# Kernel optimization log

Measured on AMD Instinct MI355X. Metric: run time of the kernel, lower is better.

## Reference

```python
import jax, jax.numpy as jnp
import numpy as np

B, T, NE, NZ, H = 64, 1024, 256, 64, 256  # batch, timesteps, n_e, n_z, encoder_hidden
SW_HID = 128  # switch MLP hidden width (hardcoded in source)


def setup_inputs() -> dict:
    key = jax.random.key(0)
    ks = jax.random.split(key, 16)
    s = 0.05
    p = lambda k, shape: (jax.random.normal(k, shape, dtype=jnp.float32) * s)
    return {
        "e_seq": jax.random.normal(ks[0], (B, T, NE), dtype=jnp.float32),
        "eps": jax.random.normal(ks[1], (B, T, NZ), dtype=jnp.float32),  # randn_like noise, precomputed
        # GRU forward direction (torch layout: weight_ih [3H, NE] order r,z,n)
        "w_ih_f": p(ks[2], (3 * H, NE)), "w_hh_f": p(ks[3], (3 * H, H)),
        "b_ih_f": jnp.zeros((3 * H,), jnp.float32), "b_hh_f": jnp.zeros((3 * H,), jnp.float32),
        # GRU backward direction
        "w_ih_b": p(ks[4], (3 * H, NE)), "w_hh_b": p(ks[5], (3 * H, H)),
        "b_ih_b": jnp.zeros((3 * H,), jnp.float32), "b_hh_b": jnp.zeros((3 * H,), jnp.float32),
        # mu / logvar heads over [B,T,2H]
        "mu_w": p(ks[6], (NZ, 2 * H)), "mu_b": jnp.zeros((NZ,), jnp.float32),
        "lv_w": p(ks[7], (NZ, 2 * H)), "lv_b": jnp.zeros((NZ,), jnp.float32),
        # switching unit: Linear(NE + 2H + NZ, 128) -> ReLU -> Linear(128,1) -> Sigmoid
        "sw_w1": p(ks[8], (SW_HID, NE + 2 * H + NZ)), "sw_b1": jnp.zeros((SW_HID,), jnp.float32),
        "sw_w2": p(ks[9], (1, SW_HID)), "sw_b2": jnp.zeros((1,), jnp.float32),
    }


def _gru_dir(x, w_ih, w_hh, b_ih, b_hh, reverse):
    # x: [B,T,NE]; torch GRU cell: r,z = sigmoid; n = tanh(x_n + r*(W_hn h + b_hn)); h' = (1-z)*n + z*h
    xp = jnp.einsum('btn,gn->btg', x, w_ih) + b_ih  # [B,T,3H] input projections, once
    xp = jnp.swapaxes(xp, 0, 1)  # [T,B,3H]
    h0 = jnp.zeros((x.shape[0], w_hh.shape[1]), x.dtype)

    def step(h, xpt):
        hp = h @ w_hh.T + b_hh
        xr, xz, xn = jnp.split(xpt, 3, axis=-1)
        hr, hz, hn = jnp.split(hp, 3, axis=-1)
        r = jax.nn.sigmoid(xr + hr)
        z = jax.nn.sigmoid(xz + hz)
        n = jnp.tanh(xn + r * hn)
        h_new = (1.0 - z) * n + z * h
        return h_new, h_new

    _, hs = jax.lax.scan(step, h0, xp, reverse=reverse)  # outputs time-aligned even when reversed
    return jnp.swapaxes(hs, 0, 1)  # [B,T,H]


def _forward(e_seq, eps, w_ih_f, w_hh_f, b_ih_f, b_hh_f, w_ih_b, w_hh_b, b_ih_b, b_hh_b,
             mu_w, mu_b, lv_w, lv_b, sw_w1, sw_b1, sw_w2, sw_b2):
    h_f = _gru_dir(e_seq, w_ih_f, w_hh_f, b_ih_f, b_hh_f, reverse=False)
    h_b = _gru_dir(e_seq, w_ih_b, w_hh_b, b_ih_b, b_hh_b, reverse=True)
    h_seq = jnp.concatenate([h_f, h_b], axis=-1)  # [B,T,2H]

    mu = h_seq @ mu_w.T + mu_b    # [B,T,NZ]
    lv = h_seq @ lv_w.T + lv_b    # [B,T,NZ]

    n_e = e_seq.shape[-1]
    h2 = h_seq.shape[-1]
    # split switch first-layer weight by input segments [e_t | h_t | z_prev]
    w1_e = sw_w1[:, :n_e]
    w1_h = sw_w1[:, n_e:n_e + h2]
    w1_z = sw_w1[:, n_e + h2:]
    # precompute e/h contributions for all t; only z_prev contribution is sequential
    pre = jnp.einsum('btn,kn->btk', e_seq, w1_e) + jnp.einsum('bth,kh->btk', h_seq, w1_h) + sw_b1  # [B,T,128]

    z_tilde = mu + jnp.exp(0.5 * lv) * eps                    # reparameterized sample [B,T,NZ]
    kl = (-0.5 * (1.0 + lv - mu * mu - jnp.exp(lv))).sum(-1)  # [B,T]

    def step(z_prev, inputs):
        pre_t, zt_t = inputs  # [B,128], [B,NZ]
        hid = jax.nn.relu(pre_t + z_prev @ w1_z.T)
        beta = jax.nn.sigmoid(hid @ sw_w2.T + sw_b2)[..., 0]  # [B]
        z_t = beta[:, None] * zt_t + (1.0 - beta[:, None]) * z_prev
        return z_t, (z_t, beta)

    z0 = jnp.zeros((e_seq.shape[0], mu.shape[-1]), e_seq.dtype)
    _, (zs, betas) = jax.lax.scan(step, z0, (jnp.swapaxes(pre, 0, 1), jnp.swapaxes(z_tilde, 0, 1)))
    z_seq = jnp.swapaxes(zs, 0, 1)     # [B,T,NZ]
    beta_seq = jnp.swapaxes(betas, 0, 1)  # [B,T]
    kl_loss = kl.mean()
    return z_seq, kl_loss, beta_seq


def reference(e_seq, eps, w_ih_f, w_hh_f, b_ih_f, b_hh_f, w_ih_b, w_hh_b, b_ih_b, b_hh_b,
              mu_w, mu_b, lv_w, lv_b, sw_w1, sw_b1, sw_w2, sw_b2):
    return _forward(e_seq, eps, w_ih_f, w_hh_f, b_ih_f, b_hh_f, w_ih_b, w_hh_b, b_ih_b, b_hh_b,
                    mu_w, mu_b, lv_w, lv_b, sw_w1, sw_b1, sw_w2, sw_b2)
```

## Files before the change

kernel.cpp:

```cpp
#include <hip/hip_runtime.h>
#include <cstdint>

typedef _Float16 half_t;
typedef _Float16 half2_t __attribute__((ext_vector_type(2)));
typedef _Float16 h8_t __attribute__((ext_vector_type(8)));
typedef float f4_t __attribute__((ext_vector_type(4)));
typedef unsigned int uint32;

static constexpr int B_ = 64, T_ = 1024;

#define DEV __device__ __forceinline__

DEV float fdot2f(half2_t a, half2_t b, float c) {
#if __has_builtin(__builtin_amdgcn_fdot2)
  return __builtin_amdgcn_fdot2(a, b, c, false);
#else
  return fmaf((float)a.x, (float)b.x, fmaf((float)a.y, (float)b.y, c));
#endif
}

DEV float fast_rcp(float x) { return __builtin_amdgcn_rcpf(x); }
DEV float sigmf(float x) { return fast_rcp(1.f + __expf(-x)); }
DEV float tanhf_(float x) { return 1.f - 2.f * fast_rcp(1.f + __expf(2.f * x)); }
DEV uint32 pack2(float a, float b) {
  half2_t h; h.x = (half_t)a; h.y = (half_t)b;
  return __builtin_bit_cast(uint32, h);
}

DEV void gload_lds16(const void* g, void* l) {
  __builtin_amdgcn_global_load_lds(
      (const __attribute__((address_space(1))) uint32*)g,
      (__attribute__((address_space(3))) uint32*)l, 16, 0, 0);
}

__global__ __launch_bounds__(256) void pack_w(
    const float* __restrict__ w_ih_f, const float* __restrict__ w_ih_b,
    const float* __restrict__ mu_w, const float* __restrict__ lv_w,
    const float* __restrict__ sw_w1,
    const float* __restrict__ w_hh_f, const float* __restrict__ w_hh_b,
    const float* __restrict__ mu_b, const float* __restrict__ lv_b,
    const float* __restrict__ sw_b1,
    uint32* __restrict__ wihf, uint32* __restrict__ wihb,
    uint32* __restrict__ wce, uint32* __restrict__ wchf, uint32* __restrict__ wchb,
    uint32* __restrict__ whh, uint32* __restrict__ w1z, float* __restrict__ biasc) {
  int id = blockIdx.x * 256 + threadIdx.x;
  if (id < 98304) { wihf[id] = pack2(w_ih_f[2*id], w_ih_f[2*id+1]); return; }
  id -= 98304;
  if (id < 98304) { wihb[id] = pack2(w_ih_b[2*id], w_ih_b[2*id+1]); return; }
  id -= 98304;
  if (id < 32768) {
    int n = id >> 7, c0 = (id & 127) * 2;
    float v0 = 0.f, v1 = 0.f;
    if (n >= 128) { const float* p = sw_w1 + (n - 128) * 832 + c0; v0 = p[0]; v1 = p[1]; }
    wce[id] = pack2(v0, v1); return;
  }
  id -= 32768;
  if (id < 32768) {
    int n = id >> 7, c0 = (id & 127) * 2;
    const float* p = (n < 64)  ? mu_w + n * 512 + c0
                   : (n < 128) ? lv_w + (n - 64) * 512 + c0
                               : sw_w1 + (n - 128) * 832 + 256 + c0;
    wchf[id] = pack2(p[0], p[1]); return;
  }
  id -= 32768;
  if (id < 32768) {
    int n = id >> 7, c0 = (id & 127) * 2;
    const float* p = (n < 64)  ? mu_w + n * 512 + 256 + c0
                   : (n < 128) ? lv_w + (n - 64) * 512 + 256 + c0
                               : sw_w1 + (n - 128) * 832 + 512 + c0;
    wchb[id] = pack2(p[0], p[1]); return;
  }
  id -= 32768;
  if (id < 196608) {
    int d = id / 98304, q = id % 98304;
    int dw = q / 512, t2 = q % 512;
    int r = t2 >> 2, pp = t2 & 3;
    int i = dw / 96, g = (dw % 96) / 32, dd = dw % 32;
    int row = 256 * g + 2 * r + i;
    int k0 = 64 * pp + 2 * dd;
    const float* w = d ? w_hh_b : w_hh_f;
    whh[id] = pack2(w[row * 256 + k0], w[row * 256 + k0 + 1]);
    return;
  }
  id -= 196608;
  if (id < 4096) {
    int j = id / 128, k2 = id % 128;
    w1z[id] = pack2(sw_w1[k2 * 832 + 768 + 2 * j], sw_w1[k2 * 832 + 768 + 2 * j + 1]);
    return;
  }
  id -= 4096;
  if (id < 256) {
    biasc[id] = (id < 64) ? mu_b[id] : (id < 128) ? lv_b[id - 64] : sw_b1[id - 128];
  }
}

template <int AF32, int ACC>
__global__ __launch_bounds__(256) void gemm_t(
    const void* __restrict__ Ap, int lda,
    const half_t* __restrict__ Bw,
    const float* __restrict__ bias,
    half_t* __restrict__ C, int ldc, int K) {
  __shared__ __align__(16) half_t smem[16384];
  half_t* As = smem;
  half_t* Bs = smem + 8192;
  const int tid = threadIdx.x;
  const int lane = tid & 63, w = tid >> 6;
  const int n0 = blockIdx.x * 128, m0 = blockIdx.y * 128;
  const int r8 = lane >> 3, c8 = lane & 7;
  f4_t acc[4][4];
  f4_t zero = {0.f, 0.f, 0.f, 0.f};
#pragma unroll
  for (int i = 0; i < 4; ++i)
#pragma unroll
    for (int j = 0; j < 4; ++j) acc[i][j] = zero;
  const int wm = (w >> 1) * 64, wn = (w & 1) * 64;
  for (int ks = 0; ks < K; ks += 64) {
    if constexpr (AF32) {
      const float* Af = (const float*)Ap;
#pragma unroll
      for (int it = 0; it < 4; ++it) {
        int c = it * 256 + tid;
        int row = c >> 3, coff = (c & 7) * 8;
        const float* ap = Af + (size_t)(m0 + row) * lda + ks + coff;
        float4 v0 = *(const float4*)ap;
        float4 v1 = *(const float4*)(ap + 4);
        uint4 u;
        u.x = pack2(v0.x, v0.y); u.y = pack2(v0.z, v0.w);
        u.z = pack2(v1.x, v1.y); u.w = pack2(v1.z, v1.w);
        *(uint4*)&As[(size_t)c * 8] = u;
      }
    } else {
      const half_t* Af = (const half_t*)Ap;
#pragma unroll
      for (int c = 0; c < 4; ++c) {
        int row = w * 32 + c * 8 + r8;
        gload_lds16(Af + (size_t)(m0 + row) * lda + ks + c8 * 8, As + (w * 4 + c) * 512);
      }
    }
#pragma unroll
    for (int c = 0; c < 4; ++c) {
      int row = w * 32 + c * 8 + r8;
      gload_lds16(Bw + (size_t)(n0 + row) * K + ks + c8 * 8, Bs + (w * 4 + c) * 512);
    }
    __syncthreads();
#pragma unroll
    for (int kk = 0; kk < 2; ++kk) {
      h8_t af[4], bf[4];
      const int ko = kk * 32 + (lane >> 4) * 8;
#pragma unroll
      for (int i = 0; i < 4; ++i) af[i] = *(const h8_t*)&As[(wm + i * 16 + (lane & 15)) * 64 + ko];
#pragma unroll
      for (int j = 0; j < 4; ++j) bf[j] = *(const h8_t*)&Bs[(wn + j * 16 + (lane & 15)) * 64 + ko];
#pragma unroll
      for (int i = 0; i < 4; ++i)
#pragma unroll
        for (int j = 0; j < 4; ++j)
          acc[i][j] = __builtin_amdgcn_mfma_f32_16x16x32_f16(af[i], bf[j], acc[i][j], 0, 0, 0);
    }
    __syncthreads();
  }
  const int cl4 = lane & 15, rl4 = lane >> 4;
#pragma unroll
  for (int j = 0; j < 4; ++j) {
    float bj = bias ? bias[n0 + wn + j * 16 + cl4] : 0.f;
#pragma unroll
    for (int i = 0; i < 4; ++i)
#pragma unroll
      for (int q = 0; q < 4; ++q) {
        int rl = wm + i * 16 + rl4 * 4 + q;
        int cc = wn + j * 16 + cl4;
        smem[rl * 128 + cc] = (half_t)(acc[i][j][q] + bj);
      }
  }
  __syncthreads();
#pragma unroll
  for (int it = 0; it < 8; ++it) {
    int idx = it * 256 + tid;
    int row = idx >> 4, colc = idx & 15;
    uint4 v = *(const uint4*)&smem[row * 128 + colc * 8];
    half_t* cp = C + (size_t)(m0 + row) * ldc + n0 + colc * 8;
    if constexpr (ACC) {
      uint4 o = *(const uint4*)cp;
      h8_t vv = __builtin_bit_cast(h8_t, v) + __builtin_bit_cast(h8_t, o);
      v = __builtin_bit_cast(uint4, vv);
    }
    *(uint4*)cp = v;
  }
}

__global__ __launch_bounds__(512, 2) void gru_rec(
    uint32* __restrict__ xp,
    const uint32* __restrict__ whh,
    const float* __restrict__ bhh_f, const float* __restrict__ bhh_b) {
  const int wg = blockIdx.x;
  const int d = wg >> 6, b = wg & 63;
  const int tid = threadIdx.x;
  const int r = tid >> 2, p = tid & 3;
  __shared__ uint32 hb[2][128];
  if (tid < 128) { hb[0][tid] = 0; hb[1][tid] = 0; }
  half2_t wv[192];
  const uint32* wp = whh + (size_t)d * 98304 + tid;
#pragma unroll
  for (int j = 0; j < 192; ++j) wv[j] = __builtin_bit_cast(half2_t, wp[j * 512]);
  const float* bhh = d ? bhh_b : bhh_f;
  float bh[6];
#pragma unroll
  for (int g = 0; g < 3; ++g) { bh[g] = bhh[256 * g + 2 * r]; bh[3 + g] = bhh[256 * g + 2 * r + 1]; }
  uint32* xpu = xp + ((size_t)d * B_ + b) * T_ * 384;
  float h0 = 0.f, h1 = 0.f;
  const int dt = d ? -1 : 1;
  int t = d ? (T_ - 1) : 0;
  uint32 xr_n = 0, xz_n = 0, xn_n = 0;
  if (p == 0) {
    const uint32* rowp = xpu + (size_t)t * 384;
    xr_n = rowp[r]; xz_n = rowp[128 + r]; xn_n = rowp[256 + r];
  }
  __syncthreads();
  for (int step = 0; step < T_; ++step) {
    const int cur = step & 1;
    const uint32 xr = xr_n, xz = xz_n, xn = xn_n;
    const int tn = (step < T_ - 1) ? (t + dt) : t;
    if (p == 0) {
      const uint32* rowp = xpu + (size_t)tn * 384;
      xr_n = rowp[r]; xz_n = rowp[128 + r]; xn_n = rowp[256 + r];
    }
    float a00 = 0, a01 = 0, a02 = 0, a10 = 0, a11 = 0, a12 = 0;
#pragma unroll
    for (int c = 0; c < 4; ++c) {
      half2_t hv[8];
#pragma unroll
      for (int e = 0; e < 8; ++e) hv[e] = __builtin_bit_cast(half2_t, hb[cur][p * 32 + c * 8 + e]);
#pragma unroll
      for (int e = 0; e < 8; ++e) {
        const int dd = c * 8 + e;
        a00 = fdot2f(wv[dd], hv[e], a00);
        a01 = fdot2f(wv[dd + 32], hv[e], a01);
        a02 = fdot2f(wv[dd + 64], hv[e], a02);
        a10 = fdot2f(wv[dd + 96], hv[e], a10);
        a11 = fdot2f(wv[dd + 128], hv[e], a11);
        a12 = fdot2f(wv[dd + 160], hv[e], a12);
      }
    }
    a00 += __shfl_xor(a00, 1); a00 += __shfl_xor(a00, 2);
    a01 += __shfl_xor(a01, 1); a01 += __shfl_xor(a01, 2);
    a02 += __shfl_xor(a02, 1); a02 += __shfl_xor(a02, 2);
    a10 += __shfl_xor(a10, 1); a10 += __shfl_xor(a10, 2);
    a11 += __shfl_xor(a11, 1); a11 += __shfl_xor(a11, 2);
    a12 += __shfl_xor(a12, 1); a12 += __shfl_xor(a12, 2);
    if (p == 0) {
      half2_t xrv = __builtin_bit_cast(half2_t, xr);
      half2_t xzv = __builtin_bit_cast(half2_t, xz);
      half2_t xnv = __builtin_bit_cast(half2_t, xn);
      float r0 = sigmf((float)xrv.x + a00 + bh[0]);
      float z0 = sigmf((float)xzv.x + a01 + bh[1]);
      float n0 = tanhf_((float)xnv.x + r0 * (a02 + bh[2]));
      h0 = (1.f - z0) * n0 + z0 * h0;
      float r1 = sigmf((float)xrv.y + a10 + bh[3]);
      float z1 = sigmf((float)xzv.y + a11 + bh[4]);
      float n1 = tanhf_((float)xnv.y + r1 * (a12 + bh[5]));
      h1 = (1.f - z1) * n1 + z1 * h1;
      uint32 ph = pack2(h0, h1);
      hb[cur ^ 1][r] = ph;
      xpu[(size_t)t * 384 + r] = ph;
    }
    __syncthreads();
    t = tn;
  }
}

__global__ __launch_bounds__(256) void zkl(const half_t* __restrict__ hp,
                                           const float* __restrict__ eps,
                                           float* __restrict__ ztil,
                                           float* __restrict__ klp) {
  const int blk = blockIdx.x, tid = threadIdx.x;
  const size_t bt = (size_t)blk * 4 + (tid >> 6);
  const int j = tid & 63;
  float mu = (float)hp[bt * 768 + j];
  float lv = (float)hp[bt * 768 + 64 + j];
  float ev = eps[bt * 64 + j];
  ztil[bt * 64 + j] = mu + __expf(0.5f * lv) * ev;
  float term = 1.f + lv - mu * mu - __expf(lv);
#pragma unroll
  for (int s = 1; s < 64; s <<= 1) term += __shfl_xor(term, s);
  __shared__ float red[4];
  if ((tid & 63) == 0) red[tid >> 6] = term;
  __syncthreads();
  if (tid == 0) klp[blk] = red[0] + red[1] + red[2] + red[3];
}

__global__ __launch_bounds__(256) void klred(const float* __restrict__ klp,
                                             float* __restrict__ out) {
  const int tid = threadIdx.x;
  float s = 0.f;
  for (int i = tid; i < 16384; i += 256) s += klp[i];
#pragma unroll
  for (int st = 1; st < 64; st <<= 1) s += __shfl_xor(s, st);
  __shared__ float red[4];
  if ((tid & 63) == 0) red[tid >> 6] = s;
  __syncthreads();
  if (tid == 0) out[0] = (red[0] + red[1] + red[2] + red[3]) * (-0.5f / 65536.f);
}

__global__ __launch_bounds__(128) void z_scan(
    const half_t* __restrict__ hp,
    const float* __restrict__ zt_arr,
    const uint32* __restrict__ w1z,
    const float* __restrict__ sw_w2, const float* __restrict__ sw_b2,
    float* __restrict__ z_out, float* __restrict__ beta_out) {
  const int b = blockIdx.x;
  const int k = threadIdx.x;
  const int w = k >> 6, lane = k & 63;
  half2_t wz[32];
#pragma unroll
  for (int j = 0; j < 32; ++j) wz[j] = __builtin_bit_cast(half2_t, w1z[j * 128 + k]);
  const float w2k = sw_w2[k];
  const float b2 = sw_b2[0];
  __shared__ uint32 zb[2][32];
  __shared__ float sred[2];
  if (k < 32) zb[0][k] = 0;
  __syncthreads();
  float zf = 0.f;
  const size_t bt0 = (size_t)b * T_;
  float pre_n = (float)hp[bt0 * 768 + 128 + k];
  float ztn = (k < 64) ? zt_arr[bt0 * 64 + k] : 0.f;
  for (int t = 0; t < T_; ++t) {
    const int cur = t & 1;
    const float pre = pre_n, zt = ztn;
    half2_t zr[32];
#pragma unroll
    for (int j = 0; j < 32; ++j) zr[j] = __builtin_bit_cast(half2_t, zb[cur][j]);
    const int tn = (t < T_ - 1) ? t + 1 : t;
    pre_n = (float)hp[(bt0 + tn) * 768 + 128 + k];
    if (k < 64) ztn = zt_arr[(bt0 + tn) * 64 + k];
    float a0 = 0, a1 = 0, a2 = 0, a3 = 0;
#pragma unroll
    for (int j = 0; j < 32; j += 4) {
      a0 = fdot2f(wz[j], zr[j], a0);
      a1 = fdot2f(wz[j + 1], zr[j + 1], a1);
      a2 = fdot2f(wz[j + 2], zr[j + 2], a2);
      a3 = fdot2f(wz[j + 3], zr[j + 3], a3);
    }
    float hid = fmaxf(pre + ((a0 + a1) + (a2 + a3)), 0.f);
    float v = hid * w2k;
#pragma unroll
    for (int s = 1; s < 64; s <<= 1) v += __shfl_xor(v, s);
    if (lane == 0) sred[w] = v;
    __syncthreads();
    const float beta = sigmf(sred[0] + sred[1] + b2);
    if (k == 0) beta_out[bt0 + t] = beta;
    if (k < 64) {
      zf = beta * zt + (1.f - beta) * zf;
      z_out[(bt0 + t) * 64 + k] = zf;
      float zo = __shfl_xor(zf, 1);
      if ((k & 1) == 0) zb[cur ^ 1][k >> 1] = pack2(zf, zo);
    }
    __syncthreads();
  }
}

extern "C" void kernel_launch(void* const* d_in, const int* in_sizes, int n_in,
                              void* d_out, int out_size, void* d_ws, size_t ws_size,
                              hipStream_t stream) {
  (void)in_sizes; (void)n_in; (void)out_size;
  const float* e_seq  = (const float*)d_in[0];
  const float* eps    = (const float*)d_in[1];
  const float* w_ih_f = (const float*)d_in[2];
  const float* w_hh_f = (const float*)d_in[3];
  const float* b_ih_f = (const float*)d_in[4];
  const float* b_hh_f = (const float*)d_in[5];
  const float* w_ih_b = (const float*)d_in[6];
  const float* w_hh_b = (const float*)d_in[7];
  const float* b_ih_b = (const float*)d_in[8];
  const float* b_hh_b = (const float*)d_in[9];
  const float* mu_w   = (const float*)d_in[10];
  const float* mu_b   = (const float*)d_in[11];
  const float* lv_w   = (const float*)d_in[12];
  const float* lv_b   = (const float*)d_in[13];
  const float* sw_w1  = (const float*)d_in[14];
  const float* sw_b1  = (const float*)d_in[15];
  const float* sw_w2  = (const float*)d_in[16];
  const float* sw_b2  = (const float*)d_in[17];

  const size_t NEED = 203310080;
  if (ws_size < NEED) return;
  char* ws = (char*)d_ws;
  half_t* xpf = (half_t*)ws;
  half_t* xpb = (half_t*)(ws + 100663296);
  half_t* hp  = xpf + 512;
  float*  ztil = (float*)(ws + 100663296);
  float*  klp  = (float*)(ws + 100663296 + 16777216);
  char* wr = ws + 201326592;
  uint32* wihf  = (uint32*)(wr);
  uint32* wihb  = (uint32*)(wr + 393216);
  uint32* wce   = (uint32*)(wr + 786432);
  uint32* wchf  = (uint32*)(wr + 917504);
  uint32* wchb  = (uint32*)(wr + 1048576);
  uint32* whhp  = (uint32*)(wr + 1179648);
  uint32* w1zp  = (uint32*)(wr + 1966080);
  float*  biasc = (float*)(wr + 1982464);

  pack_w<<<1937, 256, 0, stream>>>(w_ih_f, w_ih_b, mu_w, lv_w, sw_w1, w_hh_f, w_hh_b,
                                   mu_b, lv_b, sw_b1,
                                   wihf, wihb, wce, wchf, wchb, whhp, w1zp, biasc);
  gemm_t<1, 0><<<dim3(6, 512), 256, 0, stream>>>(e_seq, 256, (const half_t*)wihf, b_ih_f, xpf, 768, 256);
  gemm_t<1, 0><<<dim3(6, 512), 256, 0, stream>>>(e_seq, 256, (const half_t*)wihb, b_ih_b, xpb, 768, 256);
  gru_rec<<<128, 512, 0, stream>>>((uint32*)ws, whhp, b_hh_f, b_hh_b);
  gemm_t<1, 0><<<dim3(2, 512), 256, 0, stream>>>(e_seq, 256, (const half_t*)wce, biasc, hp, 768, 256);
  gemm_t<0, 1><<<dim3(2, 512), 256, 0, stream>>>(xpf, 768, (const half_t*)wchf, nullptr, hp, 768, 256);
  gemm_t<0, 1><<<dim3(2, 512), 256, 0, stream>>>(xpb, 768, (const half_t*)wchb, nullptr, hp, 768, 256);
  zkl<<<16384, 256, 0, stream>>>(hp, eps, ztil, klp);
  klred<<<1, 256, 0, stream>>>(klp, (float*)d_out + 4194304);
  z_scan<<<64, 128, 0, stream>>>(hp, ztil, w1zp, sw_w2, sw_b2, (float*)d_out, (float*)d_out + 4194305);
}
```

Measured before the change: 2.148 ms.

## Fold GRU biases, pad recurrent LDS, single-wave z_scan, trim switch GEMM

Several changes land together. The r/z hidden biases are folded into the input-projection bias, and the recurrent LDS buffer is padded and read with 128-bit loads. z_scan now runs as one 64-thread wave that handles two hidden units per lane, which removes the block barriers and the cross-wave reduction. The e_seq-to-switch GEMM now computes only the 128 nonzero columns and accumulates into hp, instead of writing zero-padded columns first. The risks are the removed barrier in z_scan, which now relies on wave-synchronous LDS ordering, and the reordered register layout for the weights.

```diff
diff --git a/kernel.cpp b/kernel.cpp
--- a/kernel.cpp
+++ b/kernel.cpp
@@ -26,6 +26,7 @@
   half2_t h; h.x = (half_t)a; h.y = (half_t)b;
   return __builtin_bit_cast(uint32, h);
 }
+DEV half2_t bch2(uint32 u) { return __builtin_bit_cast(half2_t, u); }
 
 DEV void gload_lds16(const void* g, void* l) {
   __builtin_amdgcn_global_load_lds(
@@ -38,11 +39,14 @@
     const float* __restrict__ mu_w, const float* __restrict__ lv_w,
     const float* __restrict__ sw_w1,
     const float* __restrict__ w_hh_f, const float* __restrict__ w_hh_b,
+    const float* __restrict__ b_ih_f, const float* __restrict__ b_ih_b,
+    const float* __restrict__ b_hh_f, const float* __restrict__ b_hh_b,
     const float* __restrict__ mu_b, const float* __restrict__ lv_b,
     const float* __restrict__ sw_b1,
     uint32* __restrict__ wihf, uint32* __restrict__ wihb,
-    uint32* __restrict__ wce, uint32* __restrict__ wchf, uint32* __restrict__ wchb,
-    uint32* __restrict__ whh, uint32* __restrict__ w1z, float* __restrict__ biasc) {
+    uint32* __restrict__ wchf, uint32* __restrict__ wchb, uint32* __restrict__ wce2,
+    uint32* __restrict__ whh, uint32* __restrict__ w1z,
+    float* __restrict__ biasc, float* __restrict__ biasf, float* __restrict__ biasb) {
   int id = blockIdx.x * 256 + threadIdx.x;
   if (id < 98304) { wihf[id] = pack2(w_ih_f[2*id], w_ih_f[2*id+1]); return; }
   id -= 98304;
@@ -50,13 +54,6 @@
   id -= 98304;
   if (id < 32768) {
     int n = id >> 7, c0 = (id & 127) * 2;
-    float v0 = 0.f, v1 = 0.f;
-    if (n >= 128) { const float* p = sw_w1 + (n - 128) * 832 + c0; v0 = p[0]; v1 = p[1]; }
-    wce[id] = pack2(v0, v1); return;
-  }
-  id -= 32768;
-  if (id < 32768) {
-    int n = id >> 7, c0 = (id & 127) * 2;
     const float* p = (n < 64)  ? mu_w + n * 512 + c0
                    : (n < 128) ? lv_w + (n - 64) * 512 + c0
                                : sw_w1 + (n - 128) * 832 + 256 + c0;
@@ -71,27 +68,40 @@
     wchb[id] = pack2(p[0], p[1]); return;
   }
   id -= 32768;
+  if (id < 16384) {
+    int n = id >> 7, c0 = (id & 127) * 2;
+    wce2[id] = pack2(sw_w1[n * 832 + c0], sw_w1[n * 832 + c0 + 1]); return;
+  }
+  id -= 16384;
   if (id < 196608) {
-    int d = id / 98304, q = id % 98304;
-    int dw = q / 512, t2 = q % 512;
-    int r = t2 >> 2, pp = t2 & 3;
-    int i = dw / 96, g = (dw % 96) / 32, dd = dw % 32;
-    int row = 256 * g + 2 * r + i;
-    int k0 = 64 * pp + 2 * dd;
-    const float* w = d ? w_hh_b : w_hh_f;
+    int dd = id / 98304, q = id % 98304;
+    int j = q >> 9, t2 = q & 511;
+    int rr = t2 >> 2, pp = t2 & 3;
+    int gi = j >> 5, ck = j & 31;
+    int g = gi >> 1, i = gi & 1;
+    int row = 256 * g + 2 * rr + i;
+    int k0 = pp * 64 + 2 * ck;
+    const float* w = dd ? w_hh_b : w_hh_f;
     whh[id] = pack2(w[row * 256 + k0], w[row * 256 + k0 + 1]);
     return;
   }
   id -= 196608;
   if (id < 4096) {
-    int j = id / 128, k2 = id % 128;
-    w1z[id] = pack2(sw_w1[k2 * 832 + 768 + 2 * j], sw_w1[k2 * 832 + 768 + 2 * j + 1]);
+    int j = id >> 6, kk = id & 63;
+    int row = (j < 32) ? kk : kk + 64;
+    int jj = j & 31;
+    w1z[id] = pack2(sw_w1[row * 832 + 768 + 2 * jj], sw_w1[row * 832 + 768 + 2 * jj + 1]);
     return;
   }
   id -= 4096;
   if (id < 256) {
     biasc[id] = (id < 64) ? mu_b[id] : (id < 128) ? lv_b[id - 64] : sw_b1[id - 128];
-  }
+    return;
+  }
+  id -= 256;
+  if (id < 768) { biasf[id] = b_ih_f[id] + (id < 512 ? b_hh_f[id] : 0.f); return; }
+  id -= 768;
+  if (id < 768) { biasb[id] = b_ih_b[id] + (id < 512 ? b_hh_b[id] : 0.f); return; }
 }
 
 template <int AF32, int ACC>
@@ -190,22 +200,24 @@
 
 __global__ __launch_bounds__(512, 2) void gru_rec(
     uint32* __restrict__ xp,
-    const uint32* __restrict__ whh,
+    const uint32* __restrict__ whh2,
     const float* __restrict__ bhh_f, const float* __restrict__ bhh_b) {
   const int wg = blockIdx.x;
   const int d = wg >> 6, b = wg & 63;
   const int tid = threadIdx.x;
   const int r = tid >> 2, p = tid & 3;
-  __shared__ uint32 hb[2][128];
-  if (tid < 128) { hb[0][tid] = 0; hb[1][tid] = 0; }
-  half2_t wv[192];
-  const uint32* wp = whh + (size_t)d * 98304 + tid;
-#pragma unroll
-  for (int j = 0; j < 192; ++j) wv[j] = __builtin_bit_cast(half2_t, wp[j * 512]);
+  __shared__ uint32 hb[2][144];
+  if (tid < 144) { hb[0][tid] = 0; hb[1][tid] = 0; }
+  uint32 wv[192];
+  {
+    const uint32* wp = whh2 + (size_t)d * 98304 + tid;
+#pragma unroll
+    for (int j = 0; j < 192; ++j) wv[j] = wp[(size_t)j * 512];
+#pragma unroll
+    for (int j = 0; j < 192; ++j) asm volatile("" : "+v"(wv[j]));
+  }
   const float* bhh = d ? bhh_b : bhh_f;
-  float bh[6];
-#pragma unroll
-  for (int g = 0; g < 3; ++g) { bh[g] = bhh[256 * g + 2 * r]; bh[3 + g] = bhh[256 * g + 2 * r + 1]; }
+  const float bhn0 = bhh[512 + 2 * r], bhn1 = bhh[512 + 2 * r + 1];
   uint32* xpu = xp + ((size_t)d * B_ + b) * T_ * 384;
   float h0 = 0.f, h1 = 0.f;
   const int dt = d ? -1 : 1;
@@ -215,6 +227,8 @@
     const uint32* rowp = xpu + (size_t)t * 384;
     xr_n = rowp[r]; xz_n = rowp[128 + r]; xn_n = rowp[256 + r];
   }
+  const int rdbase = p * 36;
+  const int wslice = (r >> 5) * 36 + (r & 31);
   __syncthreads();
   for (int step = 0; step < T_; ++step) {
     const int cur = step & 1;
@@ -224,43 +238,43 @@
       const uint32* rowp = xpu + (size_t)tn * 384;
       xr_n = rowp[r]; xz_n = rowp[128 + r]; xn_n = rowp[256 + r];
     }
-    float a00 = 0, a01 = 0, a02 = 0, a10 = 0, a11 = 0, a12 = 0;
+    float a00 = 0, a10 = 0, a01 = 0, a11 = 0, a02 = 0, a12 = 0;
+    const uint32* hc = &hb[cur][rdbase];
 #pragma unroll
     for (int c = 0; c < 4; ++c) {
-      half2_t hv[8];
-#pragma unroll
-      for (int e = 0; e < 8; ++e) hv[e] = __builtin_bit_cast(half2_t, hb[cur][p * 32 + c * 8 + e]);
+      uint4 u0 = *(const uint4*)(hc + c * 8);
+      uint4 u1 = *(const uint4*)(hc + c * 8 + 4);
+      uint32 hv[8] = {u0.x, u0.y, u0.z, u0.w, u1.x, u1.y, u1.z, u1.w};
 #pragma unroll
       for (int e = 0; e < 8; ++e) {
-        const int dd = c * 8 + e;
-        a00 = fdot2f(wv[dd], hv[e], a00);
-        a01 = fdot2f(wv[dd + 32], hv[e], a01);
-        a02 = fdot2f(wv[dd + 64], hv[e], a02);
-        a10 = fdot2f(wv[dd + 96], hv[e], a10);
-        a11 = fdot2f(wv[dd + 128], hv[e], a11);
-        a12 = fdot2f(wv[dd + 160], hv[e], a12);
+        const int j = c * 8 + e;
+        half2_t hh = bch2(hv[e]);
+        a00 = fdot2f(bch2(wv[j]),       hh, a00);
+        a10 = fdot2f(bch2(wv[32 + j]),  hh, a10);
+        a01 = fdot2f(bch2(wv[64 + j]),  hh, a01);
+        a11 = fdot2f(bch2(wv[96 + j]),  hh, a11);
+        a02 = fdot2f(bch2(wv[128 + j]), hh, a02);
+        a12 = fdot2f(bch2(wv[160 + j]), hh, a12);
       }
     }
     a00 += __shfl_xor(a00, 1); a00 += __shfl_xor(a00, 2);
+    a10 += __shfl_xor(a10, 1); a10 += __shfl_xor(a10, 2);
     a01 += __shfl_xor(a01, 1); a01 += __shfl_xor(a01, 2);
+    a11 += __shfl_xor(a11, 1); a11 += __shfl_xor(a11, 2);
     a02 += __shfl_xor(a02, 1); a02 += __shfl_xor(a02, 2);
-    a10 += __shfl_xor(a10, 1); a10 += __shfl_xor(a10, 2);
-    a11 += __shfl_xor(a11, 1); a11 += __shfl_xor(a11, 2);
     a12 += __shfl_xor(a12, 1); a12 += __shfl_xor(a12, 2);
     if (p == 0) {
-      half2_t xrv = __builtin_bit_cast(half2_t, xr);
-      half2_t xzv = __builtin_bit_cast(half2_t, xz);
-      half2_t xnv = __builtin_bit_cast(half2_t, xn);
-      float r0 = sigmf((float)xrv.x + a00 + bh[0]);
-      float z0 = sigmf((float)xzv.x + a01 + bh[1]);
-      float n0 = tanhf_((float)xnv.x + r0 * (a02 + bh[2]));
+      half2_t xrv = bch2(xr), xzv = bch2(xz), xnv = bch2(xn);
+      float r0 = sigmf((float)xrv.x + a00);
+      float z0 = sigmf((float)xzv.x + a01);
+      float n0 = tanhf_((float)xnv.x + r0 * (a02 + bhn0));
       h0 = (1.f - z0) * n0 + z0 * h0;
-      float r1 = sigmf((float)xrv.y + a10 + bh[3]);
-      float z1 = sigmf((float)xzv.y + a11 + bh[4]);
-      float n1 = tanhf_((float)xnv.y + r1 * (a12 + bh[5]));
+      float r1 = sigmf((float)xrv.y + a10);
+      float z1 = sigmf((float)xzv.y + a11);
+      float n1 = tanhf_((float)xnv.y + r1 * (a12 + bhn1));
       h1 = (1.f - z1) * n1 + z1 * h1;
       uint32 ph = pack2(h0, h1);
-      hb[cur ^ 1][r] = ph;
+      hb[cur ^ 1][wslice] = ph;
       xpu[(size_t)t * 384 + r] = ph;
     }
     __syncthreads();
@@ -301,7 +315,7 @@
   if (tid == 0) out[0] = (red[0] + red[1] + red[2] + red[3]) * (-0.5f / 65536.f);
 }
 
-__global__ __launch_bounds__(128) void z_scan(
+__global__ __launch_bounds__(64) void z_scan(
     const half_t* __restrict__ hp,
     const float* __restrict__ zt_arr,
     const uint32* __restrict__ w1z,
@@ -309,52 +323,53 @@
     float* __restrict__ z_out, float* __restrict__ beta_out) {
   const int b = blockIdx.x;
   const int k = threadIdx.x;
-  const int w = k >> 6, lane = k & 63;
-  half2_t wz[32];
-#pragma unroll
-  for (int j = 0; j < 32; ++j) wz[j] = __builtin_bit_cast(half2_t, w1z[j * 128 + k]);
-  const float w2k = sw_w2[k];
-  const float b2 = sw_b2[0];
+  uint32 wz[64];
+#pragma unroll
+  for (int j = 0; j < 64; ++j) wz[j] = w1z[j * 64 + k];
+#pragma unroll
+  for (int j = 0; j < 64; ++j) asm volatile("" : "+v"(wz[j]));
+  const float w2k0 = sw_w2[k], w2k1 = sw_w2[k + 64], b2 = sw_b2[0];
   __shared__ uint32 zb[2][32];
-  __shared__ float sred[2];
-  if (k < 32) zb[0][k] = 0;
+  if (k < 32) { zb[0][k] = 0; zb[1][k] = 0; }
   __syncthreads();
   float zf = 0.f;
   const size_t bt0 = (size_t)b * T_;
-  float pre_n = (float)hp[bt0 * 768 + 128 + k];
-  float ztn = (k < 64) ? zt_arr[bt0 * 64 + k] : 0.f;
+  float pre0n = (float)hp[bt0 * 768 + 128 + k];
+  float pre1n = (float)hp[bt0 * 768 + 192 + k];
+  float ztn = zt_arr[bt0 * 64 + k];
   for (int t = 0; t < T_; ++t) {
     const int cur = t & 1;
-    const float pre = pre_n, zt = ztn;
-    half2_t zr[32];
-#pragma unroll
-    for (int j = 0; j < 32; ++j) zr[j] = __builtin_bit_cast(half2_t, zb[cur][j]);
+    const float pre0 = pre0n, pre1 = pre1n, zt = ztn;
+    uint32 zr[32];
+#pragma unroll
+    for (int q = 0; q < 8; ++q) {
+      uint4 u = *(const uint4*)&zb[cur][q * 4];
+      zr[q * 4] = u.x; zr[q * 4 + 1] = u.y; zr[q * 4 + 2] = u.z; zr[q * 4 + 3] = u.w;
+    }
     const int tn = (t < T_ - 1) ? t + 1 : t;
-    pre_n = (float)hp[(bt0 + tn) * 768 + 128 + k];
-    if (k < 64) ztn = zt_arr[(bt0 + tn) * 64 + k];
+    pre0n = (float)hp[(bt0 + tn) * 768 + 128 + k];
+    pre1n = (float)hp[(bt0 + tn) * 768 + 192 + k];
+    ztn = zt_arr[(bt0 + tn) * 64 + k];
     float a0 = 0, a1 = 0, a2 = 0, a3 = 0;
 #pragma unroll
-    for (int j = 0; j < 32; j += 4) {
-      a0 = fdot2f(wz[j], zr[j], a0);
-      a1 = fdot2f(wz[j + 1], zr[j + 1], a1);
-      a2 = fdot2f(wz[j + 2], zr[j + 2], a2);
-      a3 = fdot2f(wz[j + 3], zr[j + 3], a3);
-    }
-    float hid = fmaxf(pre + ((a0 + a1) + (a2 + a3)), 0.f);
-    float v = hid * w2k;
+    for (int j = 0; j < 32; j += 2) {
+      a0 = fdot2f(bch2(wz[j]),          bch2(zr[j]),     a0);
+      a1 = fdot2f(bch2(wz[j + 1]),      bch2(zr[j + 1]), a1);
+      a2 = fdot2f(bch2(wz[32 + j]),     bch2(zr[j]),     a2);
+      a3 = fdot2f(bch2(wz[32 + j + 1]), bch2(zr[j + 1]), a3);
+    }
+    float hid0 = fmaxf(pre0 + a0 + a1, 0.f);
+    float hid1 = fmaxf(pre1 + a2 + a3, 0.f);
+    float v = fmaf(hid0, w2k0, hid1 * w2k1);
 #pragma unroll
     for (int s = 1; s < 64; s <<= 1) v += __shfl_xor(v, s);
-    if (lane == 0) sred[w] = v;
-    __syncthreads();
-    const float beta = sigmf(sred[0] + sred[1] + b2);
+    const float beta = sigmf(v + b2);
+    zf = beta * zt + (1.f - beta) * zf;
+    z_out[(bt0 + t) * 64 + k] = zf;
     if (k == 0) beta_out[bt0 + t] = beta;
-    if (k < 64) {
-      zf = beta * zt + (1.f - beta) * zf;
-      z_out[(bt0 + t) * 64 + k] = zf;
-      float zo = __shfl_xor(zf, 1);
-      if ((k & 1) == 0) zb[cur ^ 1][k >> 1] = pack2(zf, zo);
-    }
-    __syncthreads();
+    float zo = __shfl_xor(zf, 1);
+    if ((k & 1) == 0) zb[cur ^ 1][k >> 1] = pack2(zf, zo);
+    asm volatile("s_waitcnt lgkmcnt(0)" ::: "memory");
   }
 }
 
@@ -381,7 +396,7 @@
   const float* sw_w2  = (const float*)d_in[16];
   const float* sw_b2  = (const float*)d_in[17];
 
-  const size_t NEED = 203310080;
+  const size_t NEED = 201326592 + 1924096;
   if (ws_size < NEED) return;
   char* ws = (char*)d_ws;
   half_t* xpf = (half_t*)ws;
@@ -392,23 +407,26 @@
   char* wr = ws + 201326592;
   uint32* wihf  = (uint32*)(wr);
   uint32* wihb  = (uint32*)(wr + 393216);
-  uint32* wce   = (uint32*)(wr + 786432);
-  uint32* wchf  = (uint32*)(wr + 917504);
-  uint32* wchb  = (uint32*)(wr + 1048576);
-  uint32* whhp  = (uint32*)(wr + 1179648);
-  uint32* w1zp  = (uint32*)(wr + 1966080);
-  float*  biasc = (float*)(wr + 1982464);
-
-  pack_w<<<1937, 256, 0, stream>>>(w_ih_f, w_ih_b, mu_w, lv_w, sw_w1, w_hh_f, w_hh_b,
-                                   mu_b, lv_b, sw_b1,
-                                   wihf, wihb, wce, wchf, wchb, whhp, w1zp, biasc);
-  gemm_t<1, 0><<<dim3(6, 512), 256, 0, stream>>>(e_seq, 256, (const half_t*)wihf, b_ih_f, xpf, 768, 256);
-  gemm_t<1, 0><<<dim3(6, 512), 256, 0, stream>>>(e_seq, 256, (const half_t*)wihb, b_ih_b, xpb, 768, 256);
-  gru_rec<<<128, 512, 0, stream>>>((uint32*)ws, whhp, b_hh_f, b_hh_b);
-  gemm_t<1, 0><<<dim3(2, 512), 256, 0, stream>>>(e_seq, 256, (const half_t*)wce, biasc, hp, 768, 256);
-  gemm_t<0, 1><<<dim3(2, 512), 256, 0, stream>>>(xpf, 768, (const half_t*)wchf, nullptr, hp, 768, 256);
+  uint32* wchf  = (uint32*)(wr + 786432);
+  uint32* wchb  = (uint32*)(wr + 917504);
+  uint32* wce2  = (uint32*)(wr + 1048576);
+  uint32* whh2  = (uint32*)(wr + 1114112);
+  uint32* w1z2  = (uint32*)(wr + 1900544);
+  float*  biasc = (float*)(wr + 1916928);
+  float*  biasf = (float*)(wr + 1917952);
+  float*  biasb = (float*)(wr + 1921024);
+
+  pack_w<<<1879, 256, 0, stream>>>(w_ih_f, w_ih_b, mu_w, lv_w, sw_w1, w_hh_f, w_hh_b,
+                                   b_ih_f, b_ih_b, b_hh_f, b_hh_b, mu_b, lv_b, sw_b1,
+                                   wihf, wihb, wchf, wchb, wce2, whh2, w1z2,
+                                   biasc, biasf, biasb);
+  gemm_t<1, 0><<<dim3(6, 512), 256, 0, stream>>>(e_seq, 256, (const half_t*)wihf, biasf, xpf, 768, 256);
+  gemm_t<1, 0><<<dim3(6, 512), 256, 0, stream>>>(e_seq, 256, (const half_t*)wihb, biasb, xpb, 768, 256);
+  gru_rec<<<128, 512, 0, stream>>>((uint32*)ws, whh2, b_hh_f, b_hh_b);
+  gemm_t<0, 0><<<dim3(2, 512), 256, 0, stream>>>(xpf, 768, (const half_t*)wchf, biasc, hp, 768, 256);
   gemm_t<0, 1><<<dim3(2, 512), 256, 0, stream>>>(xpb, 768, (const half_t*)wchb, nullptr, hp, 768, 256);
+  gemm_t<1, 1><<<dim3(1, 512), 256, 0, stream>>>(e_seq, 256, (const half_t*)wce2, nullptr, hp + 128, 768, 256);
   zkl<<<16384, 256, 0, stream>>>(hp, eps, ztil, klp);
   klred<<<1, 256, 0, stream>>>(klp, (float*)d_out + 4194304);
-  z_scan<<<64, 128, 0, stream>>>(hp, ztil, w1zp, sw_w2, sw_b2, (float*)d_out, (float*)d_out + 4194305);
-}
+  z_scan<<<64, 64, 0, stream>>>(hp, ztil, w1z2, sw_w2, sw_b2, (float*)d_out, (float*)d_out + 4194305);
+}
```

After: 2.105 ms. 2.0% less time.
